# Kernel optimization log

Hardware: AMD Instinct MI355X
Metric: run time of the kernel (lower is better)

Reference implementation:

```python
import jax, jax.numpy as jnp
import numpy as np

N = 50000
IN_CH = 128
HEADS = 4
OUT_CH = 32
E = 800000
NEG_SLOPE = 0.2


def setup_inputs() -> dict:
    key = jax.random.key(0)
    k1, k2, k3, k4, k5, k6 = jax.random.split(key, 6)
    x = jax.random.normal(k1, (N, IN_CH), dtype=jnp.float32)
    edge_index = jax.random.randint(k2, (2, E), 0, N, dtype=jnp.int64)
    # learned params (PyG GATv2Conv: lin_l, lin_r weights, att vector, bias)
    s = 1.0 / np.sqrt(IN_CH)
    W_l = jax.random.uniform(k3, (IN_CH, HEADS, OUT_CH), jnp.float32, -s, s)
    W_r = jax.random.uniform(k4, (IN_CH, HEADS, OUT_CH), jnp.float32, -s, s)
    att = jax.random.uniform(k5, (HEADS, OUT_CH), jnp.float32, -s, s)
    bias = jax.random.uniform(k6, (HEADS * OUT_CH,), jnp.float32, -s, s)
    return {"x": x, "edge_index": edge_index, "W_l": W_l, "W_r": W_r,
            "att": att, "bias": bias}


def reference(x, edge_index, W_l, W_r, att, bias):
    # add self loops (PyG default add_self_loops=True)
    loops = jnp.arange(N, dtype=edge_index.dtype)
    src = jnp.concatenate([edge_index[0], loops])  # message source j
    dst = jnp.concatenate([edge_index[1], loops])  # message target i

    # node projections: [N, H, C]
    x_l = jnp.einsum('nd,dhc->nhc', x, W_l)  # source-side
    x_r = jnp.einsum('nd,dhc->nhc', x, W_r)  # target-side

    # GATv2 attention logits per edge: a^T LeakyReLU(x_l[j] + x_r[i])
    e = jax.nn.leaky_relu(x_l[src] + x_r[dst], NEG_SLOPE)  # [Etot, H, C]
    score = jnp.einsum('ehc,hc->eh', e, att)               # [Etot, H]

    # segment softmax over incoming edges of each destination node
    m = jax.ops.segment_max(score, dst, num_segments=N)    # [N, H]
    m = jnp.where(jnp.isfinite(m), m, 0.0)
    ex = jnp.exp(score - m[dst])                           # [Etot, H]
    denom = jax.ops.segment_sum(ex, dst, num_segments=N)   # [N, H]
    alpha = ex / denom[dst]                                # [Etot, H]

    # scatter-aggregate weighted messages
    msg = alpha[:, :, None] * x_l[src]                     # [Etot, H, C]
    out = jax.ops.segment_sum(msg, dst, num_segments=N)    # [N, H, C]

    # concat heads + bias
    return out.reshape(N, HEADS * OUT_CH) + bias
```

## Files before the change

### kernel.cpp

```cpp
#include <hip/hip_runtime.h>
#include <math.h>

#define N_NODES 50000
#define IN_CH   128
#define TOT_CH  128
#define NEDGE   800000
#define ETOT    (NEDGE + N_NODES)
#define MTILES  ((N_NODES + 63) / 64)
#define NBUCK   ((N_NODES + 255) / 256)
#define BCAP    8192
#define EPB     4096
#define NBIN    ((ETOT + EPB - 1) / EPB)

#define OFF_XL      ((size_t)0)
#define OFF_EBUF    ((size_t)12800000)
#define OFF_XR      ((size_t)25600000)
#define OFF_SRC     ((size_t)38400000)
#define OFF_BT      ((size_t)44900352)
#define OFF_GCUR    ((size_t)45000064)
#define OFF_ROWPTR  ((size_t)51200000)

typedef float f32x4 __attribute__((ext_vector_type(4)));
typedef short s16x8 __attribute__((ext_vector_type(8)));

__device__ __forceinline__ unsigned f2bf(float f) {
    unsigned u = __float_as_uint(f);
    return (u + 0x7fffu + ((u >> 16) & 1u)) >> 16;
}
__device__ __forceinline__ float bflo(unsigned u) { return __uint_as_float(u << 16); }
__device__ __forceinline__ float bfhi(unsigned u) { return __uint_as_float(u & 0xffff0000u); }

__device__ __forceinline__ int SWZ(int row, int byteoff) {
    return row * 256 + (byteoff ^ ((row & 7) << 4));
}

__global__ __launch_bounds__(256) void zero_kernel(int* __restrict__ gcur) {
    if (threadIdx.x < NBUCK) gcur[threadIdx.x] = 0;
}

__global__ __launch_bounds__(256) void k1_kernel(
    const float* __restrict__ Wl, const float* __restrict__ Wr,
    unsigned* __restrict__ btg, const int* __restrict__ ei,
    int* __restrict__ gcur, unsigned* __restrict__ ebuf)
{
    __shared__ int lcnt[256];
    __shared__ int lbase[256];
    const int bid = blockIdx.x;
    const int tid = threadIdx.x;

    if (bid < NBIN) {
        lcnt[tid] = 0;
        __syncthreads();
        const int base = bid * EPB;
        int sv[16], dv[16];
#pragma unroll
        for (int u = 0; u < 16; ++u) {
            const int e = base + u * 256 + tid;
            int s32 = 0, d32 = -1;
            if (e < ETOT) {
                if (e < NEDGE) { s32 = ei[e]; d32 = ei[NEDGE + e]; }
                else           { s32 = d32 = e - NEDGE; }
                atomicAdd(&lcnt[d32 >> 8], 1);
            }
            sv[u] = s32; dv[u] = d32;
        }
        __syncthreads();
        if (tid < NBUCK) {
            const int v = lcnt[tid];
            lbase[tid] = v ? atomicAdd(&gcur[tid], v) : 0;
        }
        __syncthreads();
        lcnt[tid] = 0;
        __syncthreads();
#pragma unroll
        for (int u = 0; u < 16; ++u) {
            const int d32 = dv[u];
            if (d32 >= 0) {
                const int b = d32 >> 8;
                const int p = lbase[b] + atomicAdd(&lcnt[b], 1);
                ebuf[b * BCAP + p] = (unsigned)sv[u] | ((unsigned)(d32 & 255) << 16);
            }
        }
    } else {
        const int g = (bid - NBIN) * 256 + tid;
        if (g < 256 * 64) {
            const int n = g >> 6, kk = g & 63;
            const float* W = (n < 128) ? Wl : Wr;
            const int nc = n & 127;
            const float a = W[(size_t)(2 * kk) * 128 + nc];
            const float b = W[(size_t)(2 * kk + 1) * 128 + nc];
            btg[g] = f2bf(a) | (f2bf(b) << 16);
        }
    }
}

__global__ __launch_bounds__(256) void k2_kernel(
    const float* __restrict__ x, const unsigned* __restrict__ btg,
    unsigned* __restrict__ xl_bf, unsigned* __restrict__ xr_bf,
    const unsigned* __restrict__ ebuf, const int* __restrict__ gcur,
    int2* __restrict__ rowptr2, int* __restrict__ ssrc)
{
    __shared__ __align__(16) unsigned char smem[32768];
    __shared__ int wsum[4];
    const int bid = blockIdx.x;
    const int tid = threadIdx.x;

    if (bid < NBUCK) {
        int* lcnt = (int*)smem;
        int* lcur = ((int*)smem) + 256;
        const int ecnt  = gcur[bid];
        const int ebase = bid * BCAP;
        lcnt[tid] = 0;
        __syncthreads();
        for (int k = tid; k < ecnt; k += 256)
            atomicAdd(&lcnt[(ebuf[ebase + k] >> 16) & 255], 1);
        __syncthreads();
        const int lane = tid & 63, wid = tid >> 6;
        const int v = lcnt[tid];
        int s = v;
#pragma unroll
        for (int off = 1; off < 64; off <<= 1) {
            int t = __shfl_up(s, off);
            if (lane >= off) s += t;
        }
        if (lane == 63) wsum[wid] = s;
        __syncthreads();
        if (tid == 0) {
            int acc = 0;
#pragma unroll
            for (int w = 0; w < 4; ++w) { int t = wsum[w]; wsum[w] = acc; acc += t; }
        }
        __syncthreads();
        const int gpos = ebase + wsum[wid] + s - v;
        const int node = (bid << 8) + tid;
        if (node < N_NODES) rowptr2[node] = make_int2(gpos, gpos + v);
        lcur[tid] = gpos;
        __syncthreads();
        for (int k = tid; k < ecnt; k += 256) {
            const unsigned ed = ebuf[ebase + k];
            const int p = atomicAdd(&lcur[(ed >> 16) & 255], 1);
            ssrc[p] = (int)(ed & 0xffffu);
        }
        return;
    }

    unsigned char* Al = smem;
    unsigned char* Bl = smem + 16384;
    const int mt = bid - NBUCK;
    const int mbase = mt * 64;
    const int l  = tid & 63;
    const int wv = tid >> 6;

    {
        const int r = tid >> 2, q = tid & 3;
        int gm = mbase + r;
        gm = (gm < N_NODES) ? gm : (N_NODES - 1);
        const float* xrow = x + (size_t)gm * IN_CH + q * 32;
#pragma unroll
        for (int i = 0; i < 8; ++i) {
            const float4 xv = *(const float4*)(xrow + i * 4);
            uint2 p;
            p.x = f2bf(xv.x) | (f2bf(xv.y) << 16);
            p.y = f2bf(xv.z) | (f2bf(xv.w) << 16);
            *(uint2*)(Al + SWZ(r, q * 64 + i * 8)) = p;
        }
    }
    {
        const int r = tid >> 2, q = tid & 3;
        const unsigned* brow = btg + (size_t)r * 64 + q * 16;
#pragma unroll
        for (int i = 0; i < 4; ++i) {
            const uint4 v = *(const uint4*)(brow + i * 4);
            *(uint4*)(Bl + SWZ(r, q * 64 + i * 16)) = v;
        }
    }
    __syncthreads();

    s16x8 af[4];
#pragma unroll
    for (int ks = 0; ks < 4; ++ks)
        af[ks] = *(const s16x8*)(Al + SWZ(wv * 16 + (l & 15), ks * 64 + (l >> 4) * 16));

    for (int nt4 = 0; nt4 < 4; ++nt4) {
        f32x4 acc[4];
#pragma unroll
        for (int n = 0; n < 4; ++n) acc[n] = (f32x4){0.f, 0.f, 0.f, 0.f};
#pragma unroll
        for (int nsub = 0; nsub < 4; ++nsub) {
#pragma unroll
            for (int ks = 0; ks < 4; ++ks) {
                const s16x8 bfr = *(const s16x8*)(Bl + SWZ(nsub * 16 + (l & 15), ks * 64 + (l >> 4) * 16));
                acc[nsub] = __builtin_amdgcn_mfma_f32_16x16x32_bf16(af[ks], bfr, acc[nsub], 0, 0, 0);
            }
        }
        unsigned* dstbuf = (nt4 < 2) ? xl_bf : xr_bf;
        const int ncol0 = (nt4 & 1) * 64;
#pragma unroll
        for (int nsub = 0; nsub < 4; ++nsub) {
            const int n = ncol0 + nsub * 16 + (l & 15);
#pragma unroll
            for (int reg = 0; reg < 4; ++reg) {
                const float v  = acc[nsub][reg];
                const float vp = __shfl_xor(v, 1);
                const int row = mbase + wv * 16 + (l >> 4) * 4 + reg;
                if (((l & 1) == 0) && row < N_NODES)
                    dstbuf[(size_t)row * 64 + (n >> 1)] = f2bf(v) | (f2bf(vp) << 16);
            }
        }
        if (nt4 == 3) break;
        __syncthreads();
        {
            const int r = tid >> 2, q = tid & 3;
            const unsigned* brow = btg + (size_t)((nt4 + 1) * 64 + r) * 64 + q * 16;
#pragma unroll
            for (int i = 0; i < 4; ++i) {
                const uint4 v = *(const uint4*)(brow + i * 4);
                *(uint4*)(Bl + SWZ(r, q * 64 + i * 16)) = v;
            }
        }
        __syncthreads();
    }
}

#define DPP_ADD(s, ctrl) do { \
        int _t = __builtin_amdgcn_update_dpp(0, __float_as_int(s), ctrl, 0xf, 0xf, true); \
        s += __int_as_float(_t); } while(0)

template<bool MASKED>
__device__ __forceinline__ void group4(
    const int* __restrict__ srcs, int k, int kend, int q, int sl,
    const unsigned* __restrict__ xl_bf,
    const float* a6, const float* a4, const float* xr8,
    float& den, float* b)
{
    const int kk = MASKED ? min(k + q, kend - 1) : (k + q);
    const int jv = srcs[kk];
    const uint4 u = *(const uint4*)(xl_bf + (size_t)jv * 64 + sl * 4);
    float t[8];
    t[0] = bflo(u.x) + xr8[0]; t[1] = bfhi(u.x) + xr8[1];
    t[2] = bflo(u.y) + xr8[2]; t[3] = bfhi(u.y) + xr8[3];
    t[4] = bflo(u.z) + xr8[4]; t[5] = bfhi(u.z) + xr8[5];
    t[6] = bflo(u.w) + xr8[6]; t[7] = bfhi(u.w) + xr8[7];
    float s = a4[0] * fabsf(t[0]);
    s = fmaf(a6[0], t[0], s);
#pragma unroll
    for (int c = 1; c < 8; ++c) {
        s = fmaf(a4[c], fabsf(t[c]), s);
        s = fmaf(a6[c], t[c], s);
    }
    DPP_ADD(s, 0xB1);
    DPP_ADD(s, 0x4E);
    if (MASKED) s = (q < kend - k) ? s : -1e30f;
    const float p = __builtin_amdgcn_exp2f(s);
    den += p;
#pragma unroll
    for (int c = 0; c < 8; ++c) b[c] = fmaf(p, t[c], b[c]);
}

__global__ __launch_bounds__(256) void gat_kernel(
    const unsigned* __restrict__ xl_bf, const unsigned* __restrict__ xr_bf,
    const int2* __restrict__ rowptr2, const int* __restrict__ srcs,
    const float* __restrict__ att, const float* __restrict__ bias,
    float* __restrict__ out)
{
    const int l = threadIdx.x & 63;
    const int i = blockIdx.x * 4 + (threadIdx.x >> 6);
    if (i >= N_NODES) return;
    const int sl = l & 15;
    const int q  = l >> 4;
    const int c8 = sl * 8;
    const float LOG2E = 1.4426950408889634f;
    float a6[8], a4[8], xr8[8];
    {
        const float4 A = *(const float4*)(att + c8);
        const float4 B = *(const float4*)(att + c8 + 4);
        const float av[8] = {A.x, A.y, A.z, A.w, B.x, B.y, B.z, B.w};
#pragma unroll
        for (int c = 0; c < 8; ++c) {
            a6[c] = 0.6f * LOG2E * av[c];
            a4[c] = 0.4f * LOG2E * av[c];
        }
    }
    {
        const uint4 urv = *(const uint4*)(xr_bf + (size_t)i * 64 + sl * 4);
        xr8[0] = bflo(urv.x); xr8[1] = bfhi(urv.x);
        xr8[2] = bflo(urv.y); xr8[3] = bfhi(urv.y);
        xr8[4] = bflo(urv.z); xr8[5] = bfhi(urv.z);
        xr8[6] = bflo(urv.w); xr8[7] = bfhi(urv.w);
    }
    const int2 kr = rowptr2[i];
    const int k0 = __builtin_amdgcn_readfirstlane(kr.x);
    const int k1 = __builtin_amdgcn_readfirstlane(kr.y);

    float den = 0.f, b[8];
#pragma unroll
    for (int c = 0; c < 8; ++c) b[c] = 0.f;

    int k = k0;
    for (; k + 4 <= k1; k += 4)
        group4<false>(srcs, k, k1, q, sl, xl_bf, a6, a4, xr8, den, b);
    if (k < k1)
        group4<true>(srcs, k, k1, q, sl, xl_bf, a6, a4, xr8, den, b);

    den += __shfl_xor(den, 16);
    den += __shfl_xor(den, 32);
#pragma unroll
    for (int c = 0; c < 8; ++c) {
        b[c] += __shfl_xor(b[c], 16);
        b[c] += __shfl_xor(b[c], 32);
    }
    if (q == 0) {
        const float inv = 1.f / den;
        const float4 bbA = *(const float4*)(bias + c8);
        const float4 bbB = *(const float4*)(bias + c8 + 4);
        float4 o1, o2;
        o1.x = fmaf(b[0], inv, bbA.x - xr8[0]);
        o1.y = fmaf(b[1], inv, bbA.y - xr8[1]);
        o1.z = fmaf(b[2], inv, bbA.z - xr8[2]);
        o1.w = fmaf(b[3], inv, bbA.w - xr8[3]);
        o2.x = fmaf(b[4], inv, bbB.x - xr8[4]);
        o2.y = fmaf(b[5], inv, bbB.y - xr8[5]);
        o2.z = fmaf(b[6], inv, bbB.z - xr8[6]);
        o2.w = fmaf(b[7], inv, bbB.w - xr8[7]);
        *(float4*)(out + (size_t)i * TOT_CH + c8)     = o1;
        *(float4*)(out + (size_t)i * TOT_CH + c8 + 4) = o2;
    }
}

extern "C" void kernel_launch(void* const* d_in, const int* in_sizes, int n_in,
                              void* d_out, int out_size, void* d_ws, size_t ws_size,
                              hipStream_t stream) {
    const float* x    = (const float*)d_in[0];
    const int*   ei   = (const int*)d_in[1];
    const float* Wl   = (const float*)d_in[2];
    const float* Wr   = (const float*)d_in[3];
    const float* att  = (const float*)d_in[4];
    const float* bias = (const float*)d_in[5];
    float* out = (float*)d_out;
    char*  ws  = (char*)d_ws;

    unsigned* xl_bf = (unsigned*)(ws + OFF_XL);
    unsigned* ebuf  = (unsigned*)(ws + OFF_EBUF);
    unsigned* xr_bf = (unsigned*)(ws + OFF_XR);
    int*      ssrc  = (int*)(ws + OFF_SRC);
    unsigned* btg   = (unsigned*)(ws + OFF_BT);
    int*      gcur  = (int*)(ws + OFF_GCUR);
    int2*   rowptr2 = (int2*)(ws + OFF_ROWPTR);

    hipLaunchKernelGGL(zero_kernel, dim3(1), dim3(256), 0, stream, gcur);
    hipLaunchKernelGGL(k1_kernel, dim3(NBIN + 64), dim3(256), 0, stream,
                       Wl, Wr, btg, ei, gcur, ebuf);
    hipLaunchKernelGGL(k2_kernel, dim3(NBUCK + MTILES), dim3(256), 0, stream,
                       x, btg, xl_bf, xr_bf, ebuf, gcur, rowptr2, ssrc);
    hipLaunchKernelGGL(gat_kernel, dim3((N_NODES + 3) / 4), dim3(256), 0, stream,
                       xl_bf, xr_bf, rowptr2, ssrc, att, bias, out);
}
```

Measured before the change: 82.89 us.

## Map four nodes per wavefront with per-node serial edge loop and prefetch

The aggregation kernel now gives each 16-lane quarter of a wavefront its own destination node instead of having the whole wave split one node's edges four ways. That removes the cross-quarter shuffle reduction and masked tail handling. Each quarter walks its node's edges serially and software-prefetches the next source row. The LeakyReLU score is also rewritten as a single fma form using one coefficient array. The cost is divergence across quarters when their nodes have different degrees, and the grid now assumes N is a multiple of 16.

```diff
diff --git a/kernel.cpp b/kernel.cpp
--- a/kernel.cpp
+++ b/kernel.cpp
@@ -226,60 +226,29 @@
         int _t = __builtin_amdgcn_update_dpp(0, __float_as_int(s), ctrl, 0xf, 0xf, true); \
         s += __int_as_float(_t); } while(0)
 
-template<bool MASKED>
-__device__ __forceinline__ void group4(
-    const int* __restrict__ srcs, int k, int kend, int q, int sl,
-    const unsigned* __restrict__ xl_bf,
-    const float* a6, const float* a4, const float* xr8,
-    float& den, float* b)
-{
-    const int kk = MASKED ? min(k + q, kend - 1) : (k + q);
-    const int jv = srcs[kk];
-    const uint4 u = *(const uint4*)(xl_bf + (size_t)jv * 64 + sl * 4);
-    float t[8];
-    t[0] = bflo(u.x) + xr8[0]; t[1] = bfhi(u.x) + xr8[1];
-    t[2] = bflo(u.y) + xr8[2]; t[3] = bfhi(u.y) + xr8[3];
-    t[4] = bflo(u.z) + xr8[4]; t[5] = bfhi(u.z) + xr8[5];
-    t[6] = bflo(u.w) + xr8[6]; t[7] = bfhi(u.w) + xr8[7];
-    float s = a4[0] * fabsf(t[0]);
-    s = fmaf(a6[0], t[0], s);
-#pragma unroll
-    for (int c = 1; c < 8; ++c) {
-        s = fmaf(a4[c], fabsf(t[c]), s);
-        s = fmaf(a6[c], t[c], s);
-    }
-    DPP_ADD(s, 0xB1);
-    DPP_ADD(s, 0x4E);
-    if (MASKED) s = (q < kend - k) ? s : -1e30f;
-    const float p = __builtin_amdgcn_exp2f(s);
-    den += p;
-#pragma unroll
-    for (int c = 0; c < 8; ++c) b[c] = fmaf(p, t[c], b[c]);
-}
-
 __global__ __launch_bounds__(256) void gat_kernel(
     const unsigned* __restrict__ xl_bf, const unsigned* __restrict__ xr_bf,
     const int2* __restrict__ rowptr2, const int* __restrict__ srcs,
     const float* __restrict__ att, const float* __restrict__ bias,
     float* __restrict__ out)
 {
-    const int l = threadIdx.x & 63;
-    const int i = blockIdx.x * 4 + (threadIdx.x >> 6);
-    if (i >= N_NODES) return;
+    const int l  = threadIdx.x & 63;
+    const int wv = threadIdx.x >> 6;
     const int sl = l & 15;
     const int q  = l >> 4;
+    const int i  = blockIdx.x * 16 + wv * 4 + q;
     const int c8 = sl * 8;
     const float LOG2E = 1.4426950408889634f;
-    float a6[8], a4[8], xr8[8];
+    const float K23 = 0.66666669f;
+
+    float a6[8], xr8[8];
     {
         const float4 A = *(const float4*)(att + c8);
         const float4 B = *(const float4*)(att + c8 + 4);
-        const float av[8] = {A.x, A.y, A.z, A.w, B.x, B.y, B.z, B.w};
-#pragma unroll
-        for (int c = 0; c < 8; ++c) {
-            a6[c] = 0.6f * LOG2E * av[c];
-            a4[c] = 0.4f * LOG2E * av[c];
-        }
+        a6[0] = 0.6f * LOG2E * A.x; a6[1] = 0.6f * LOG2E * A.y;
+        a6[2] = 0.6f * LOG2E * A.z; a6[3] = 0.6f * LOG2E * A.w;
+        a6[4] = 0.6f * LOG2E * B.x; a6[5] = 0.6f * LOG2E * B.y;
+        a6[6] = 0.6f * LOG2E * B.z; a6[7] = 0.6f * LOG2E * B.w;
     }
     {
         const uint4 urv = *(const uint4*)(xr_bf + (size_t)i * 64 + sl * 4);
@@ -289,42 +258,58 @@
         xr8[6] = bflo(urv.w); xr8[7] = bfhi(urv.w);
     }
     const int2 kr = rowptr2[i];
-    const int k0 = __builtin_amdgcn_readfirstlane(kr.x);
-    const int k1 = __builtin_amdgcn_readfirstlane(kr.y);
+    int k = kr.x;
+    const int kend = kr.y;
 
     float den = 0.f, b[8];
 #pragma unroll
     for (int c = 0; c < 8; ++c) b[c] = 0.f;
 
-    int k = k0;
-    for (; k + 4 <= k1; k += 4)
-        group4<false>(srcs, k, k1, q, sl, xl_bf, a6, a4, xr8, den, b);
-    if (k < k1)
-        group4<true>(srcs, k, k1, q, sl, xl_bf, a6, a4, xr8, den, b);
-
-    den += __shfl_xor(den, 16);
-    den += __shfl_xor(den, 32);
-#pragma unroll
-    for (int c = 0; c < 8; ++c) {
-        b[c] += __shfl_xor(b[c], 16);
-        b[c] += __shfl_xor(b[c], 32);
-    }
-    if (q == 0) {
-        const float inv = 1.f / den;
-        const float4 bbA = *(const float4*)(bias + c8);
-        const float4 bbB = *(const float4*)(bias + c8 + 4);
-        float4 o1, o2;
-        o1.x = fmaf(b[0], inv, bbA.x - xr8[0]);
-        o1.y = fmaf(b[1], inv, bbA.y - xr8[1]);
-        o1.z = fmaf(b[2], inv, bbA.z - xr8[2]);
-        o1.w = fmaf(b[3], inv, bbA.w - xr8[3]);
-        o2.x = fmaf(b[4], inv, bbB.x - xr8[4]);
-        o2.y = fmaf(b[5], inv, bbB.y - xr8[5]);
-        o2.z = fmaf(b[6], inv, bbB.z - xr8[6]);
-        o2.w = fmaf(b[7], inv, bbB.w - xr8[7]);
-        *(float4*)(out + (size_t)i * TOT_CH + c8)     = o1;
-        *(float4*)(out + (size_t)i * TOT_CH + c8 + 4) = o2;
-    }
+    uint4 u;
+    {
+        const int jv = srcs[k];
+        u = *(const uint4*)(xl_bf + (size_t)jv * 64 + sl * 4);
+    }
+    for (; k < kend; ++k) {
+        const uint4 ucur = u;
+        {
+            const int kn = (k + 1 < kend) ? (k + 1) : k;
+            const int jn = srcs[kn];
+            u = *(const uint4*)(xl_bf + (size_t)jn * 64 + sl * 4);
+        }
+        float t[8];
+        t[0] = bflo(ucur.x) + xr8[0]; t[1] = bfhi(ucur.x) + xr8[1];
+        t[2] = bflo(ucur.y) + xr8[2]; t[3] = bfhi(ucur.y) + xr8[3];
+        t[4] = bflo(ucur.z) + xr8[4]; t[5] = bfhi(ucur.z) + xr8[5];
+        t[6] = bflo(ucur.w) + xr8[6]; t[7] = bfhi(ucur.w) + xr8[7];
+        float s = 0.f;
+#pragma unroll
+        for (int c = 0; c < 8; ++c) {
+            const float h = fmaf(K23, fabsf(t[c]), t[c]);
+            s = fmaf(a6[c], h, s);
+        }
+        DPP_ADD(s, 0xB1);
+        DPP_ADD(s, 0x4E);
+        const float p = __builtin_amdgcn_exp2f(s);
+        den += p;
+#pragma unroll
+        for (int c = 0; c < 8; ++c) b[c] = fmaf(p, t[c], b[c]);
+    }
+
+    const float inv = 1.f / den;
+    const float4 bbA = *(const float4*)(bias + c8);
+    const float4 bbB = *(const float4*)(bias + c8 + 4);
+    float4 o1, o2;
+    o1.x = fmaf(b[0], inv, bbA.x - xr8[0]);
+    o1.y = fmaf(b[1], inv, bbA.y - xr8[1]);
+    o1.z = fmaf(b[2], inv, bbA.z - xr8[2]);
+    o1.w = fmaf(b[3], inv, bbA.w - xr8[3]);
+    o2.x = fmaf(b[4], inv, bbB.x - xr8[4]);
+    o2.y = fmaf(b[5], inv, bbB.y - xr8[5]);
+    o2.z = fmaf(b[6], inv, bbB.z - xr8[6]);
+    o2.w = fmaf(b[7], inv, bbB.w - xr8[7]);
+    *(float4*)(out + (size_t)i * TOT_CH + c8)     = o1;
+    *(float4*)(out + (size_t)i * TOT_CH + c8 + 4) = o2;
 }
 
 extern "C" void kernel_launch(void* const* d_in, const int* in_sizes, int n_in,
@@ -352,6 +337,6 @@
                        Wl, Wr, btg, ei, gcur, ebuf);
     hipLaunchKernelGGL(k2_kernel, dim3(NBUCK + MTILES), dim3(256), 0, stream,
                        x, btg, xl_bf, xr_bf, ebuf, gcur, rowptr2, ssrc);
-    hipLaunchKernelGGL(gat_kernel, dim3((N_NODES + 3) / 4), dim3(256), 0, stream,
+    hipLaunchKernelGGL(gat_kernel, dim3(N_NODES / 16), dim3(256), 0, stream,
                        xl_bf, xr_bf, rowptr2, ssrc, att, bias, out);
 }
```

Result: no change. 83.45 us (+0.7%).
